# Performance work log

Hardware: AMD Instinct MI355X
Metric: run time of the kernel (lower is better)

The kernel has to match this reference:

```python
import jax, jax.numpy as jnp
import numpy as np

NUM_EXPERTS = 4
MLP_RATIO = 4


def setup_inputs() -> dict:
    key = jax.random.key(0)
    k1, k2, k3, k4, k5, k6 = jax.random.split(key, 6)
    B, N, D = 4, 4096, 1024
    OUT = 1024
    H = D * MLP_RATIO
    x = jax.random.normal(k1, (B, N, D), dtype=jnp.float32)
    expert_mask = jax.random.randint(k2, (B, N), 0, NUM_EXPERTS, dtype=jnp.int64)
    w1 = jax.random.normal(k3, (H, D), dtype=jnp.float32) * 0.02
    b1 = jax.random.normal(k4, (H,), dtype=jnp.float32) * 0.02
    w2 = jax.random.normal(k5, (OUT, H), dtype=jnp.float32) * 0.02
    b2 = jax.random.normal(k6, (OUT,), dtype=jnp.float32) * 0.02
    return {"x": x, "expert_mask": expert_mask, "w1": w1, "b1": b1, "w2": w2, "b2": b2}


def reference(x, expert_mask, w1, b1, w2, b2):
    # x: [B, N, D]; expert_mask: [B, N] in [0, NUM_EXPERTS)
    D = x.shape[-1]
    OUT = w2.shape[0]
    E = NUM_EXPERTS
    y = jnp.zeros(x.shape[:-1] + (OUT,), dtype=x.dtype)
    for e in range(E):
        shift = E - 1 - e  # expert E-1 uses full width
        d_in = D >> shift
        d_hid = d_in * MLP_RATIO
        d_out = OUT >> shift
        # nested slice of shared weights
        h = jax.nn.gelu(
            jnp.einsum('bnd,hd->bnh', x[..., :d_in], w1[:d_hid, :d_in]) + b1[:d_hid],
            approximate=False,
        )
        ye = jnp.einsum('bnh,oh->bno', h, w2[:d_out, :d_hid]) + b2[:d_out]
        ye = jnp.pad(ye, ((0, 0), (0, 0), (0, OUT - d_out)))  # zero-fill unused dims
        y = y + jnp.where((expert_mask == e)[..., None], ye, jnp.zeros((), dtype=x.dtype))
    return y
```

## Files before the change

kernel.cpp:

```cpp
#include <hip/hip_runtime.h>
#include <hip/hip_bf16.h>

#define T_TOK 16384
#define DMODEL 1024
#define HDIM 4096
#define OUTD 1024

typedef __attribute__((ext_vector_type(8))) short short8_t;
typedef __attribute__((ext_vector_type(4))) float f32x4;

#define WS_COUNTS_OFF 0
#define WS_HBASE_OFF 64
#define WS_XBASE_OFF 96
#define WS_LIST_OFF 128
#define WS_XC_OFF   ((size_t)1 << 20)
#define WS_W1BF_OFF ((size_t)34 << 20)
#define WS_W2BF_OFF ((size_t)43 << 20)
#define WS_HBUF_OFF ((size_t)52 << 20)

#define W1N (HDIM * DMODEL)
#define W2N (OUTD * HDIM)

__device__ __forceinline__ short f2bf(float f) {
    union { float f; unsigned u; } x; x.f = f;
    unsigned r = x.u + 0x7FFFu + ((x.u >> 16) & 1u);
    return (short)(r >> 16);
}

__device__ __forceinline__ float gelu_exact(float v) {
    return 0.5f * v * (1.0f + erff(v * 0.7071067811865476f));
}

__device__ __forceinline__ void conv8(const float* __restrict__ s, short* __restrict__ d) {
    const float4* s4 = (const float4*)s;
    float4 f0 = s4[0], f1 = s4[1];
    short8_t v;
    v[0] = f2bf(f0.x); v[1] = f2bf(f0.y); v[2] = f2bf(f0.z); v[3] = f2bf(f0.w);
    v[4] = f2bf(f1.x); v[5] = f2bf(f1.y); v[6] = f2bf(f1.z); v[7] = f2bf(f1.w);
    *(short8_t*)d = v;
}

__device__ __forceinline__ void gl_lds16(const short* g, short* lds) {
    __builtin_amdgcn_global_load_lds(
        (const __attribute__((address_space(1))) void*)g,
        (__attribute__((address_space(3))) void*)lds, 16, 0, 0);
}

__global__ void k_convert(const float* __restrict__ w1, const float* __restrict__ w2,
                          short* __restrict__ w1bf, short* __restrict__ w2bf) {
    size_t elem = ((size_t)blockIdx.x * blockDim.x + threadIdx.x) * 8;
    if (elem < (size_t)W1N) {
        conv8(w1 + elem, w1bf + elem);
    } else {
        size_t o = elem - W1N; conv8(w2 + o, w2bf + o);
    }
}

__global__ void k_init(int* counts) {
    if (threadIdx.x < 4) counts[threadIdx.x] = 0;
}

__global__ void k_build(const int* __restrict__ mask, int* counts, int* list) {
    __shared__ int hcnt[4], hb[4], hpos[4];
    int tid = threadIdx.x;
    if (tid < 4) hcnt[tid] = 0;
    __syncthreads();
    int t = blockIdx.x * 256 + tid;
    int e = mask[t] & 3;
    atomicAdd(&hcnt[e], 1);
    __syncthreads();
    if (tid < 4) { hb[tid] = atomicAdd(&counts[tid], hcnt[tid]); hpos[tid] = 0; }
    __syncthreads();
    int p = atomicAdd(&hpos[e], 1);
    list[e * T_TOK + hb[e] + p] = t;
}

__global__ void k_bases(const int* counts, unsigned long long* hbase,
                        unsigned long long* xbase) {
    if (threadIdx.x == 0) {
        unsigned long long ha = 0, xa = 0;
        for (int e = 0; e < 4; ++e) {
            hbase[e] = ha; xbase[e] = xa;
            int d_in = 128 << e;
            ha += (unsigned long long)counts[e] * (unsigned long long)(d_in * 4);
            xa += (unsigned long long)counts[e] * (unsigned long long)d_in;
        }
    }
}

__global__ void k_xgather(const float* __restrict__ x, const int* __restrict__ counts,
                          const unsigned long long* __restrict__ xbase,
                          const int* __restrict__ list, short* __restrict__ xc) {
    const int e = blockIdx.y;
    const int d_in = 128 << e;
    const int cnt = counts[e];
    const size_t nel = (size_t)cnt * d_in;
    const int* lst = list + e * T_TOK;
    short* dst = xc + xbase[e];
    for (size_t idx = ((size_t)blockIdx.x * 256 + threadIdx.x) * 8; idx < nel;
         idx += (size_t)gridDim.x * 256 * 8) {
        int row = (int)(idx >> (7 + e));
        int col = (int)(idx & (d_in - 1));
        int tok = lst[row];
        conv8(x + (size_t)tok * DMODEL + col, dst + idx);
    }
}

__global__ __launch_bounds__(256) void k_pass1(
    const short* __restrict__ xc, const short* __restrict__ w1bf,
    const float* __restrict__ b1,
    const int* __restrict__ counts, const unsigned long long* __restrict__ hbase,
    const unsigned long long* __restrict__ xbase, short* __restrict__ hbuf)
{
    int by = blockIdx.y;
    int e, nt;
    if (by < 32)      { e = 3; nt = by; }
    else if (by < 48) { e = 2; nt = by - 32; }
    else if (by < 56) { e = 1; nt = by - 48; }
    else              { e = 0; nt = by - 56; }
    const int d_in = 128 << e;
    const int d_hid = d_in * 4;
    const int n0 = nt * 128;
    const int cnt = counts[e];
    const unsigned long long hb = hbase[e];
    const short* xe = xc + xbase[e];

    __shared__ short Ab[64 * 64];
    __shared__ short Bb[128 * 64];

    const int tid = threadIdx.x;
    const int lane = tid & 63;
    const int w = tid >> 6;
    const int l3 = lane >> 3;
    const int ch = lane & 7;
    const int wm = (w & 1) * 32;
    const int wn = (w >> 1) * 64;

    for (int m0 = blockIdx.x * 64; m0 < cnt; m0 += 64 * 64) {
        int rA[2];
#pragma unroll
        for (int j = 0; j < 2; ++j) {
            int rr = m0 + j * 32 + w * 8 + l3;
            rA[j] = (rr >= cnt) ? (cnt - 1) : rr;
        }

        f32x4 acc[2][4];
#pragma unroll
        for (int i = 0; i < 2; ++i)
#pragma unroll
            for (int j = 0; j < 4; ++j)
                acc[i][j] = (f32x4){0.f, 0.f, 0.f, 0.f};

        for (int k0 = 0; k0 < d_in; k0 += 64) {
#pragma unroll
            for (int j = 0; j < 2; ++j) {
                int r = j * 32 + w * 8 + l3;
                gl_lds16(xe + (size_t)rA[j] * d_in + k0 + ((ch ^ (r & 7)) << 3),
                         &Ab[(j * 32 + w * 8) * 64]);
            }
#pragma unroll
            for (int j = 0; j < 4; ++j) {
                int r = j * 32 + w * 8 + l3;
                gl_lds16(w1bf + (size_t)(n0 + r) * DMODEL + k0 + ((ch ^ (r & 7)) << 3),
                         &Bb[(j * 32 + w * 8) * 64]);
            }
            __syncthreads();
#pragma unroll
            for (int kk = 0; kk < 2; ++kk) {
                short8_t af[2], bfr[4];
                const int q = (lane >> 4) + kk * 4;
#pragma unroll
                for (int mt = 0; mt < 2; ++mt) {
                    int row = wm + mt * 16 + (lane & 15);
                    af[mt] = *(const short8_t*)&Ab[((row << 3) | (q ^ (row & 7))) << 3];
                }
#pragma unroll
                for (int ntn = 0; ntn < 4; ++ntn) {
                    int row = wn + ntn * 16 + (lane & 15);
                    bfr[ntn] = *(const short8_t*)&Bb[((row << 3) | (q ^ (row & 7))) << 3];
                }
#pragma unroll
                for (int mt = 0; mt < 2; ++mt)
#pragma unroll
                    for (int ntn = 0; ntn < 4; ++ntn)
                        acc[mt][ntn] = __builtin_amdgcn_mfma_f32_16x16x32_bf16(
                            af[mt], bfr[ntn], acc[mt][ntn], 0, 0, 0);
            }
            __syncthreads();
        }

        const int cl = lane & 15;
        const int qr = lane >> 4;
#pragma unroll
        for (int ntn = 0; ntn < 4; ++ntn) {
            int col = n0 + wn + ntn * 16 + cl;
            float bias = b1[col];
#pragma unroll
            for (int mt = 0; mt < 2; ++mt) {
#pragma unroll
                for (int r = 0; r < 4; ++r) {
                    int row = wm + mt * 16 + qr * 4 + r;
                    if (m0 + row < cnt) {
                        float v = acc[mt][ntn][r] + bias;
                        hbuf[hb + (unsigned long long)(m0 + row) * d_hid + col] =
                            f2bf(gelu_exact(v));
                    }
                }
            }
        }
    }
}

__global__ __launch_bounds__(256) void k_pass2(
    const short* __restrict__ hbuf, const short* __restrict__ w2bf,
    const float* __restrict__ b2,
    const int* __restrict__ counts, const unsigned long long* __restrict__ hbase,
    const int* __restrict__ list, float* __restrict__ y)
{
    int by = blockIdx.y;
    int e, nt;
    if (by < 8)       { e = 3; nt = by; }
    else if (by < 12) { e = 2; nt = by - 8; }
    else if (by < 14) { e = 1; nt = by - 12; }
    else              { e = 0; nt = 0; }
    const int d_in = 128 << e;
    const int d_hid = d_in * 4;
    const int n0 = nt * 128;
    const int cnt = counts[e];
    const int* lst = list + e * T_TOK;
    const unsigned long long hb = hbase[e];

    __shared__ short Ab[2 * 64 * 64];
    __shared__ short Bb[2 * 128 * 64];

    const int tid = threadIdx.x;
    const int lane = tid & 63;
    const int w = tid >> 6;
    const int l3 = lane >> 3;
    const int ch = lane & 7;
    const int wm = (w & 1) * 32;
    const int wn = (w >> 1) * 64;

    for (int m0 = blockIdx.x * 64; m0 < cnt; m0 += 64 * 64) {
        int rA[2];
#pragma unroll
        for (int j = 0; j < 2; ++j) {
            int rr = m0 + j * 32 + w * 8 + l3;
            rA[j] = (rr >= cnt) ? (cnt - 1) : rr;
        }

        f32x4 acc[2][4];
#pragma unroll
        for (int i = 0; i < 2; ++i)
#pragma unroll
            for (int j = 0; j < 4; ++j)
                acc[i][j] = (f32x4){0.f, 0.f, 0.f, 0.f};

        const int ks = d_hid >> 6;
#pragma unroll
        for (int j = 0; j < 2; ++j) {
            int r = j * 32 + w * 8 + l3;
            gl_lds16(hbuf + hb + (size_t)rA[j] * d_hid + ((ch ^ (r & 7)) << 3),
                     &Ab[(j * 32 + w * 8) * 64]);
        }
#pragma unroll
        for (int j = 0; j < 4; ++j) {
            int r = j * 32 + w * 8 + l3;
            gl_lds16(w2bf + (size_t)(n0 + r) * HDIM + ((ch ^ (r & 7)) << 3),
                     &Bb[(j * 32 + w * 8) * 64]);
        }
        for (int kt = 0; kt < ks; ++kt) {
            const int p = kt & 1;
            __syncthreads();
            if (kt + 1 < ks) {
                const int kn = (kt + 1) << 6;
                const int qb = 1 - p;
#pragma unroll
                for (int j = 0; j < 2; ++j) {
                    int r = j * 32 + w * 8 + l3;
                    gl_lds16(hbuf + hb + (size_t)rA[j] * d_hid + kn + ((ch ^ (r & 7)) << 3),
                             &Ab[(qb * 4096) + (j * 32 + w * 8) * 64]);
                }
#pragma unroll
                for (int j = 0; j < 4; ++j) {
                    int r = j * 32 + w * 8 + l3;
                    gl_lds16(w2bf + (size_t)(n0 + r) * HDIM + kn + ((ch ^ (r & 7)) << 3),
                             &Bb[(qb * 8192) + (j * 32 + w * 8) * 64]);
                }
            }
            const short* Ap = &Ab[p * 4096];
            const short* Bp = &Bb[p * 8192];
#pragma unroll
            for (int kk = 0; kk < 2; ++kk) {
                short8_t af[2], bfr[4];
                const int q = (lane >> 4) + kk * 4;
#pragma unroll
                for (int mt = 0; mt < 2; ++mt) {
                    int row = wm + mt * 16 + (lane & 15);
                    af[mt] = *(const short8_t*)&Ap[((row << 3) | (q ^ (row & 7))) << 3];
                }
#pragma unroll
                for (int ntn = 0; ntn < 4; ++ntn) {
                    int row = wn + ntn * 16 + (lane & 15);
                    bfr[ntn] = *(const short8_t*)&Bp[((row << 3) | (q ^ (row & 7))) << 3];
                }
#pragma unroll
                for (int mt = 0; mt < 2; ++mt)
#pragma unroll
                    for (int ntn = 0; ntn < 4; ++ntn)
                        acc[mt][ntn] = __builtin_amdgcn_mfma_f32_16x16x32_bf16(
                            af[mt], bfr[ntn], acc[mt][ntn], 0, 0, 0);
            }
        }
        __syncthreads();

        const int cl = lane & 15;
        const int qr = lane >> 4;
#pragma unroll
        for (int ntn = 0; ntn < 4; ++ntn) {
            int col = n0 + wn + ntn * 16 + cl;
            float bias = b2[col];
#pragma unroll
            for (int mt = 0; mt < 2; ++mt) {
#pragma unroll
                for (int r = 0; r < 4; ++r) {
                    int row = wm + mt * 16 + qr * 4 + r;
                    if (m0 + row < cnt) {
                        int tok = lst[m0 + row];
                        y[(size_t)tok * OUTD + col] = acc[mt][ntn][r] + bias;
                    }
                }
            }
        }
    }
}

extern "C" void kernel_launch(void* const* d_in, const int* in_sizes, int n_in,
                              void* d_out, int out_size, void* d_ws, size_t ws_size,
                              hipStream_t stream) {
    const float* x  = (const float*)d_in[0];
    const int* mask = (const int*)d_in[1];
    const float* w1 = (const float*)d_in[2];
    const float* b1 = (const float*)d_in[3];
    const float* w2 = (const float*)d_in[4];
    const float* b2 = (const float*)d_in[5];
    float* y = (float*)d_out;

    char* ws = (char*)d_ws;
    int* counts = (int*)(ws + WS_COUNTS_OFF);
    unsigned long long* hbase = (unsigned long long*)(ws + WS_HBASE_OFF);
    unsigned long long* xbase = (unsigned long long*)(ws + WS_XBASE_OFF);
    int* list = (int*)(ws + WS_LIST_OFF);
    short* xc   = (short*)(ws + WS_XC_OFF);
    short* w1bf = (short*)(ws + WS_W1BF_OFF);
    short* w2bf = (short*)(ws + WS_W2BF_OFF);
    short* hbuf = (short*)(ws + WS_HBUF_OFF);

    hipMemsetAsync(d_out, 0, (size_t)out_size * sizeof(float), stream);

    k_convert<<<(W1N + W2N) / 8 / 256, 256, 0, stream>>>(w1, w2, w1bf, w2bf);

    k_init<<<1, 64, 0, stream>>>(counts);
    k_build<<<T_TOK / 256, 256, 0, stream>>>(mask, counts, list);
    k_bases<<<1, 1, 0, stream>>>(counts, hbase, xbase);
    k_xgather<<<dim3(128, 4), 256, 0, stream>>>(x, counts, xbase, list, xc);

    k_pass1<<<dim3(64, 60), 256, 0, stream>>>(xc, w1bf, b1, counts, hbase, xbase, hbuf);
    k_pass2<<<dim3(64, 15), 256, 0, stream>>>(hbuf, w2bf, b2, counts, hbase, list, y);
}
```

Before: 377.2 us.

## Replace direct global-to-LDS loads with register-staged two-deep prefetch in both GEMMs

Both GEMM kernels stop using global_load_lds and instead load tiles into registers, two k-steps ahead, then write them to a single-buffered LDS tile before computing. The aim is to hide global memory latency behind MFMA work, which pass1 previously did not overlap at all. In exchange it uses more VGPRs, may lower occupancy, and adds extra LDS write instructions plus four barriers per two k-steps. It also assumes ks is even, which holds since d_in is at least 128.

New measurement: 1.025 ms. 172% more time.

```diff
diff --git a/kernel.cpp b/kernel.cpp
--- a/kernel.cpp
+++ b/kernel.cpp
@@ -38,12 +38,6 @@
     v[0] = f2bf(f0.x); v[1] = f2bf(f0.y); v[2] = f2bf(f0.z); v[3] = f2bf(f0.w);
     v[4] = f2bf(f1.x); v[5] = f2bf(f1.y); v[6] = f2bf(f1.z); v[7] = f2bf(f1.w);
     *(short8_t*)d = v;
-}
-
-__device__ __forceinline__ void gl_lds16(const short* g, short* lds) {
-    __builtin_amdgcn_global_load_lds(
-        (const __attribute__((address_space(1))) void*)g,
-        (__attribute__((address_space(3))) void*)lds, 16, 0, 0);
 }
 
 __global__ void k_convert(const float* __restrict__ w1, const float* __restrict__ w2,
@@ -105,6 +99,43 @@
         conv8(x + (size_t)tok * DMODEL + col, dst + idx);
     }
 }
+
+
+#define LOAD_SET(rs) do { \
+    rs[0] = *(const int4*)ga0; rs[1] = *(const int4*)ga1; \
+    rs[2] = *(const int4*)gb0; rs[3] = *(const int4*)gb1; \
+    rs[4] = *(const int4*)gb2; rs[5] = *(const int4*)gb3; \
+    ga0 += 64; ga1 += 64; gb0 += 64; gb1 += 64; gb2 += 64; gb3 += 64; \
+} while (0)
+
+#define WRITE_SET(rs) do { \
+    *la0 = rs[0]; *la1 = rs[1]; \
+    *lb0 = rs[2]; *lb1 = rs[3]; *lb2 = rs[4]; *lb3 = rs[5]; \
+} while (0)
+
+#define COMPUTE(NACC) do { \
+    _Pragma("unroll") \
+    for (int kk = 0; kk < 2; ++kk) { \
+        short8_t af[2], bfr[4]; \
+        const int q = (lane >> 4) + kk * 4; \
+        _Pragma("unroll") \
+        for (int mt = 0; mt < 2; ++mt) { \
+            int row = wm + mt * 16 + (lane & 15); \
+            af[mt] = *(const short8_t*)&Ab[((row << 3) | (q ^ (row & 7))) << 3]; \
+        } \
+        _Pragma("unroll") \
+        for (int ntn = 0; ntn < 4; ++ntn) { \
+            int row = wn + ntn * 16 + (lane & 15); \
+            bfr[ntn] = *(const short8_t*)&Bb[((row << 3) | (q ^ (row & 7))) << 3]; \
+        } \
+        _Pragma("unroll") \
+        for (int mt = 0; mt < 2; ++mt) \
+            _Pragma("unroll") \
+            for (int ntn = 0; ntn < 4; ++ntn) \
+                acc[mt][ntn] = __builtin_amdgcn_mfma_f32_16x16x32_bf16( \
+                    af[mt], bfr[ntn], acc[mt][ntn], 0, 0, 0); \
+    } \
+} while (0)
 
 __global__ __launch_bounds__(256) void k_pass1(
     const short* __restrict__ xc, const short* __restrict__ w1bf,
@@ -136,12 +167,27 @@
     const int wm = (w & 1) * 32;
     const int wn = (w >> 1) * 64;
 
+    int4* la0 = (int4*)&Ab[(0 * 32 + w * 8) * 64 + lane * 8];
+    int4* la1 = (int4*)&Ab[(1 * 32 + w * 8) * 64 + lane * 8];
+    int4* lb0 = (int4*)&Bb[(0 * 32 + w * 8) * 64 + lane * 8];
+    int4* lb1 = (int4*)&Bb[(1 * 32 + w * 8) * 64 + lane * 8];
+    int4* lb2 = (int4*)&Bb[(2 * 32 + w * 8) * 64 + lane * 8];
+    int4* lb3 = (int4*)&Bb[(3 * 32 + w * 8) * 64 + lane * 8];
+
     for (int m0 = blockIdx.x * 64; m0 < cnt; m0 += 64 * 64) {
-        int rA[2];
-#pragma unroll
-        for (int j = 0; j < 2; ++j) {
-            int rr = m0 + j * 32 + w * 8 + l3;
-            rA[j] = (rr >= cnt) ? (cnt - 1) : rr;
+        const short *ga0, *ga1, *gb0, *gb1, *gb2, *gb3;
+        {
+            int r0r = 0 * 32 + w * 8 + l3, r1r = 1 * 32 + w * 8 + l3;
+            int rr0 = m0 + r0r; if (rr0 >= cnt) rr0 = cnt - 1;
+            int rr1 = m0 + r1r; if (rr1 >= cnt) rr1 = cnt - 1;
+            ga0 = xe + (size_t)rr0 * d_in + ((ch ^ (r0r & 7)) << 3);
+            ga1 = xe + (size_t)rr1 * d_in + ((ch ^ (r1r & 7)) << 3);
+            int b0r = 0 * 32 + w * 8 + l3, b1r = 1 * 32 + w * 8 + l3;
+            int b2r = 2 * 32 + w * 8 + l3, b3r = 3 * 32 + w * 8 + l3;
+            gb0 = w1bf + (size_t)(n0 + b0r) * DMODEL + ((ch ^ (b0r & 7)) << 3);
+            gb1 = w1bf + (size_t)(n0 + b1r) * DMODEL + ((ch ^ (b1r & 7)) << 3);
+            gb2 = w1bf + (size_t)(n0 + b2r) * DMODEL + ((ch ^ (b2r & 7)) << 3);
+            gb3 = w1bf + (size_t)(n0 + b3r) * DMODEL + ((ch ^ (b3r & 7)) << 3);
         }
 
         f32x4 acc[2][4];
@@ -151,41 +197,20 @@
             for (int j = 0; j < 4; ++j)
                 acc[i][j] = (f32x4){0.f, 0.f, 0.f, 0.f};
 
-        for (int k0 = 0; k0 < d_in; k0 += 64) {
-#pragma unroll
-            for (int j = 0; j < 2; ++j) {
-                int r = j * 32 + w * 8 + l3;
-                gl_lds16(xe + (size_t)rA[j] * d_in + k0 + ((ch ^ (r & 7)) << 3),
-                         &Ab[(j * 32 + w * 8) * 64]);
-            }
-#pragma unroll
-            for (int j = 0; j < 4; ++j) {
-                int r = j * 32 + w * 8 + l3;
-                gl_lds16(w1bf + (size_t)(n0 + r) * DMODEL + k0 + ((ch ^ (r & 7)) << 3),
-                         &Bb[(j * 32 + w * 8) * 64]);
-            }
-            __syncthreads();
-#pragma unroll
-            for (int kk = 0; kk < 2; ++kk) {
-                short8_t af[2], bfr[4];
-                const int q = (lane >> 4) + kk * 4;
-#pragma unroll
-                for (int mt = 0; mt < 2; ++mt) {
-                    int row = wm + mt * 16 + (lane & 15);
-                    af[mt] = *(const short8_t*)&Ab[((row << 3) | (q ^ (row & 7))) << 3];
-                }
-#pragma unroll
-                for (int ntn = 0; ntn < 4; ++ntn) {
-                    int row = wn + ntn * 16 + (lane & 15);
-                    bfr[ntn] = *(const short8_t*)&Bb[((row << 3) | (q ^ (row & 7))) << 3];
-                }
-#pragma unroll
-                for (int mt = 0; mt < 2; ++mt)
-#pragma unroll
-                    for (int ntn = 0; ntn < 4; ++ntn)
-                        acc[mt][ntn] = __builtin_amdgcn_mfma_f32_16x16x32_bf16(
-                            af[mt], bfr[ntn], acc[mt][ntn], 0, 0, 0);
-            }
+        const int ks = d_in >> 6;
+        int4 r0[6], r1[6];
+        LOAD_SET(r0);
+        LOAD_SET(r1);
+        for (int kt = 0; kt < ks; kt += 2) {
+            WRITE_SET(r0);
+            if (kt + 2 < ks) LOAD_SET(r0);
+            __syncthreads();
+            COMPUTE(2);
+            __syncthreads();
+            WRITE_SET(r1);
+            if (kt + 3 < ks) LOAD_SET(r1);
+            __syncthreads();
+            COMPUTE(2);
             __syncthreads();
         }
 
@@ -230,8 +255,8 @@
     const int* lst = list + e * T_TOK;
     const unsigned long long hb = hbase[e];
 
-    __shared__ short Ab[2 * 64 * 64];
-    __shared__ short Bb[2 * 128 * 64];
+    __shared__ short Ab[64 * 64];
+    __shared__ short Bb[128 * 64];
 
     const int tid = threadIdx.x;
     const int lane = tid & 63;
@@ -241,12 +266,27 @@
     const int wm = (w & 1) * 32;
     const int wn = (w >> 1) * 64;
 
+    int4* la0 = (int4*)&Ab[(0 * 32 + w * 8) * 64 + lane * 8];
+    int4* la1 = (int4*)&Ab[(1 * 32 + w * 8) * 64 + lane * 8];
+    int4* lb0 = (int4*)&Bb[(0 * 32 + w * 8) * 64 + lane * 8];
+    int4* lb1 = (int4*)&Bb[(1 * 32 + w * 8) * 64 + lane * 8];
+    int4* lb2 = (int4*)&Bb[(2 * 32 + w * 8) * 64 + lane * 8];
+    int4* lb3 = (int4*)&Bb[(3 * 32 + w * 8) * 64 + lane * 8];
+
     for (int m0 = blockIdx.x * 64; m0 < cnt; m0 += 64 * 64) {
-        int rA[2];
-#pragma unroll
-        for (int j = 0; j < 2; ++j) {
-            int rr = m0 + j * 32 + w * 8 + l3;
-            rA[j] = (rr >= cnt) ? (cnt - 1) : rr;
+        const short *ga0, *ga1, *gb0, *gb1, *gb2, *gb3;
+        {
+            int r0r = 0 * 32 + w * 8 + l3, r1r = 1 * 32 + w * 8 + l3;
+            int rr0 = m0 + r0r; if (rr0 >= cnt) rr0 = cnt - 1;
+            int rr1 = m0 + r1r; if (rr1 >= cnt) rr1 = cnt - 1;
+            ga0 = hbuf + hb + (size_t)rr0 * d_hid + ((ch ^ (r0r & 7)) << 3);
+            ga1 = hbuf + hb + (size_t)rr1 * d_hid + ((ch ^ (r1r & 7)) << 3);
+            int b0r = 0 * 32 + w * 8 + l3, b1r = 1 * 32 + w * 8 + l3;
+            int b2r = 2 * 32 + w * 8 + l3, b3r = 3 * 32 + w * 8 + l3;
+            gb0 = w2bf + (size_t)(n0 + b0r) * HDIM + ((ch ^ (b0r & 7)) << 3);
+            gb1 = w2bf + (size_t)(n0 + b1r) * HDIM + ((ch ^ (b1r & 7)) << 3);
+            gb2 = w2bf + (size_t)(n0 + b2r) * HDIM + ((ch ^ (b2r & 7)) << 3);
+            gb3 = w2bf + (size_t)(n0 + b3r) * HDIM + ((ch ^ (b3r & 7)) << 3);
         }
 
         f32x4 acc[2][4];
@@ -257,62 +297,21 @@
                 acc[i][j] = (f32x4){0.f, 0.f, 0.f, 0.f};
 
         const int ks = d_hid >> 6;
-#pragma unroll
-        for (int j = 0; j < 2; ++j) {
-            int r = j * 32 + w * 8 + l3;
-            gl_lds16(hbuf + hb + (size_t)rA[j] * d_hid + ((ch ^ (r & 7)) << 3),
-                     &Ab[(j * 32 + w * 8) * 64]);
-        }
-#pragma unroll
-        for (int j = 0; j < 4; ++j) {
-            int r = j * 32 + w * 8 + l3;
-            gl_lds16(w2bf + (size_t)(n0 + r) * HDIM + ((ch ^ (r & 7)) << 3),
-                     &Bb[(j * 32 + w * 8) * 64]);
-        }
-        for (int kt = 0; kt < ks; ++kt) {
-            const int p = kt & 1;
-            __syncthreads();
-            if (kt + 1 < ks) {
-                const int kn = (kt + 1) << 6;
-                const int qb = 1 - p;
-#pragma unroll
-                for (int j = 0; j < 2; ++j) {
-                    int r = j * 32 + w * 8 + l3;
-                    gl_lds16(hbuf + hb + (size_t)rA[j] * d_hid + kn + ((ch ^ (r & 7)) << 3),
-                             &Ab[(qb * 4096) + (j * 32 + w * 8) * 64]);
-                }
-#pragma unroll
-                for (int j = 0; j < 4; ++j) {
-                    int r = j * 32 + w * 8 + l3;
-                    gl_lds16(w2bf + (size_t)(n0 + r) * HDIM + kn + ((ch ^ (r & 7)) << 3),
-                             &Bb[(qb * 8192) + (j * 32 + w * 8) * 64]);
-                }
-            }
-            const short* Ap = &Ab[p * 4096];
-            const short* Bp = &Bb[p * 8192];
-#pragma unroll
-            for (int kk = 0; kk < 2; ++kk) {
-                short8_t af[2], bfr[4];
-                const int q = (lane >> 4) + kk * 4;
-#pragma unroll
-                for (int mt = 0; mt < 2; ++mt) {
-                    int row = wm + mt * 16 + (lane & 15);
-                    af[mt] = *(const short8_t*)&Ap[((row << 3) | (q ^ (row & 7))) << 3];
-                }
-#pragma unroll
-                for (int ntn = 0; ntn < 4; ++ntn) {
-                    int row = wn + ntn * 16 + (lane & 15);
-                    bfr[ntn] = *(const short8_t*)&Bp[((row << 3) | (q ^ (row & 7))) << 3];
-                }
-#pragma unroll
-                for (int mt = 0; mt < 2; ++mt)
-#pragma unroll
-                    for (int ntn = 0; ntn < 4; ++ntn)
-                        acc[mt][ntn] = __builtin_amdgcn_mfma_f32_16x16x32_bf16(
-                            af[mt], bfr[ntn], acc[mt][ntn], 0, 0, 0);
-            }
-        }
-        __syncthreads();
+        int4 r0[6], r1[6];
+        LOAD_SET(r0);
+        LOAD_SET(r1);
+        for (int kt = 0; kt < ks; kt += 2) {
+            WRITE_SET(r0);
+            if (kt + 2 < ks) LOAD_SET(r0);
+            __syncthreads();
+            COMPUTE(2);
+            __syncthreads();
+            WRITE_SET(r1);
+            if (kt + 3 < ks) LOAD_SET(r1);
+            __syncthreads();
+            COMPUTE(2);
+            __syncthreads();
+        }
 
         const int cl = lane & 15;
         const int qr = lane >> 4;
```
